# Kernel optimization log

Hardware: AMD Instinct MI355X
Metric: run time of the kernel (lower is better)

The kernel has to match this reference:

```python
import jax, jax.numpy as jnp
import numpy as np

B, S, H, M = 4, 4096, 2048, 64
LN_EPS = 1e-5


def setup_inputs() -> dict:
    key = jax.random.key(0)
    ks = jax.random.split(key, 12)
    rn = lambda i, shape, s: (jax.random.normal(ks[i], shape, jnp.float32) * s)
    return {
        "current_hidden_states": rn(0, (B, S, H), 1.0),
        "layer_input": rn(1, (B, S, H), 1.0),
        "memory_keys": rn(2, (M, H), 0.02),
        "memory_values": rn(3, (M, H), 0.02),
        "Wq": rn(4, (H, H), 0.02), "bq": jnp.zeros((H,), jnp.float32),
        "Wk": rn(5, (H, H), 0.02), "bk": jnp.zeros((H,), jnp.float32),
        "Wv": rn(6, (H, H), 0.02), "bv": jnp.zeros((H,), jnp.float32),
        "Wg1": rn(7, (H // 2, 2 * H), 0.02), "bg1": jnp.zeros((H // 2,), jnp.float32),
        "Wg2": rn(8, (1, H // 2), 0.02), "bg2": jnp.zeros((1,), jnp.float32),
        "ln_gamma": jnp.ones((H,), jnp.float32),
        "ln_beta": jnp.zeros((H,), jnp.float32),
        "usage_count": jnp.zeros((M,), jnp.int32),
        "timestamp": jnp.zeros((M,), jnp.int32),
    }


def _linear(x, W, b):
    # torch nn.Linear: y = x @ W.T + b, W is [out, in]
    return jnp.einsum("...i,oi->...o", x, W) + b


def reference(current_hidden_states, layer_input, memory_keys, memory_values,
              Wq, bq, Wk, bk, Wv, bv, Wg1, bg1, Wg2, bg2, ln_gamma, ln_beta,
              usage_count, timestamp):
    q = _linear(layer_input, Wq, bq)              # [B,S,H]
    k = _linear(current_hidden_states, Wk, bk)    # [B,S,H]
    v = _linear(current_hidden_states, Wv, bv)    # [B,S,H]

    # memory retrieval: softmax over the 64 memory slots
    attn = jax.nn.softmax(jnp.einsum("bsh,mh->bsm", q, memory_keys), axis=-1)
    retrieved = jnp.einsum("bsm,mh->bsh", attn, memory_values)

    # gated fusion
    combined = jnp.concatenate([layer_input, retrieved], axis=-1)  # [B,S,2H]
    g_hidden = jax.nn.relu(_linear(combined, Wg1, bg1))
    reuse_gate = jax.nn.sigmoid(_linear(g_hidden, Wg2, bg2))       # [B,S,1]
    fused = (1.0 - reuse_gate) * current_hidden_states + reuse_gate * retrieved

    # LayerNorm (dropout p=0 -> identity)
    mu = jnp.mean(fused, axis=-1, keepdims=True)
    var = jnp.mean(jnp.square(fused - mu), axis=-1, keepdims=True)
    out = (fused - mu) * jax.lax.rsqrt(var + LN_EPS) * ln_gamma + ln_beta

    # sequential argmin-scatter memory update (torch no_grad loop -> lax.scan)
    key_batch = k.mean(axis=1)    # [B,H]
    value_batch = v.mean(axis=1)  # [B,H]

    def step(carry, kv):
        mk, mv, uc, ts = carry
        ki, vi = kv
        score = uc.astype(jnp.float32) + ts.astype(jnp.float32) * 0.1
        idx = jnp.argmin(score)
        mk = mk.at[idx].set(ki)
        mv = mv.at[idx].set(vi)
        uc = uc.at[idx].add(1)
        ts = ts.at[idx].set(ts.max() + 1)
        return (mk, mv, uc, ts), None

    (mk, mv, uc, ts), _ = jax.lax.scan(
        step, (memory_keys, memory_values, usage_count, timestamp),
        (key_batch, value_batch))

    return out, reuse_gate, mk, mv, uc, ts
```

## Files before the change

### kernel.cpp

```cpp
#include <hip/hip_runtime.h>
#include <hip/hip_bf16.h>
#include <stdint.h>

typedef __bf16 bf16;
typedef __bf16 bf16x8 __attribute__((ext_vector_type(8)));
typedef __bf16 bf16x4 __attribute__((ext_vector_type(4)));
typedef float  f32x4  __attribute__((ext_vector_type(4)));

#define DI __device__ __forceinline__

constexpr int ROWS = 4 * 4096;
constexpr int HH   = 2048;
constexpr int MM   = 64;
constexpr int NHID = 1024;
constexpr int NC   = 1152;

constexpr size_t O_OUT  = 0;
constexpr size_t O_GATE = (size_t)ROWS * HH;
constexpr size_t O_MK   = O_GATE + ROWS;
constexpr size_t O_MV   = O_MK + (size_t)MM * HH;
constexpr size_t O_UC   = O_MV + (size_t)MM * HH;
constexpr size_t O_TS   = O_UC + MM;

constexpr size_t WS_XLB  = 0;
constexpr size_t WS_C    = WS_XLB + (size_t)ROWS * HH * 2;
constexpr size_t WS_BMAT = WS_C + (size_t)ROWS * NC * 2;
constexpr size_t WS_WQT  = WS_BMAT + (size_t)NC * HH * 2;
constexpr size_t WS_W1B  = WS_WQT + (size_t)HH * HH * 2;
constexpr size_t WS_MKP  = WS_W1B + (size_t)NHID * HH * 2;
constexpr size_t WS_MVP  = WS_MKP + (size_t)128 * HH * 2;
constexpr size_t WS_Q2T  = WS_MVP + (size_t)128 * HH * 2;
constexpr size_t WS_PF   = WS_Q2T + (size_t)NHID * MM * 2;
constexpr size_t WS_Q2F  = WS_PF + (size_t)MM * HH * 4;
constexpr size_t WS_CVEC = WS_Q2F + (size_t)MM * NHID * 4;
constexpr size_t WS_XBAR = WS_CVEC + 64 * 4;
constexpr size_t WS_KB   = WS_XBAR + (size_t)4 * HH * 4;
constexpr size_t WS_VB   = WS_KB + (size_t)4 * HH * 4;
constexpr size_t WS_MVT  = WS_VB + (size_t)4 * HH * 4;

DI void gload16(const void* g, void* l) {
    __builtin_amdgcn_global_load_lds((__attribute__((address_space(1))) void*)g,
                                     (__attribute__((address_space(3))) void*)l,
                                     16, 0, 0);
}

DI bf16x8 cvt8(f32x4 a, f32x4 b) {
    bf16x8 v;
    v[0]=(bf16)a[0]; v[1]=(bf16)a[1]; v[2]=(bf16)a[2]; v[3]=(bf16)a[3];
    v[4]=(bf16)b[0]; v[5]=(bf16)b[1]; v[6]=(bf16)b[2]; v[7]=(bf16)b[3];
    return v;
}

DI float wave_sum(float v) {
#pragma unroll
    for (int off = 32; off; off >>= 1) v += __shfl_xor(v, off);
    return v;
}

template <bool SPLITK, bool REMAP>
__global__ __launch_bounds__(256)
void gemm_bt(const bf16* __restrict__ A, int lda,
             const bf16* __restrict__ Bt, int ldb,
             void* __restrict__ Cv, int ldc,
             int Mmax, int kit)
{
    __shared__ __align__(16) bf16 As[128 * 64];
    __shared__ __align__(16) bf16 Bs[128 * 64];
    const int tid  = threadIdx.x;
    const int wid  = tid >> 6, lane = tid & 63;
    int bx, by;
    if (REMAP) {
        int bid = blockIdx.x;
        int xcd = bid & 7, loc = bid >> 3;
        bx = xcd * 16 + loc / 9;
        by = loc % 9;
    } else { bx = blockIdx.x; by = blockIdx.y; }
    const int m0   = bx * 128, n0 = by * 128;
    const int wr   = wid >> 1, wc = wid & 1;
    const int kt0  = blockIdx.z * kit;
    const int srow  = lane >> 3;
    const int sslot = (lane & 7) ^ srow;

    f32x4 acc[4][4] = {};

    for (int kt = kt0; kt < kt0 + kit; ++kt) {
        const bf16* Ak = A + (size_t)kt * 64;
        const bf16* Bk = Bt + (size_t)kt * 64;
#pragma unroll
        for (int c = 0; c < 4; ++c) {
            int ch  = wid * 4 + c;
            int row = ch * 8 + srow;
            gload16(Ak + (size_t)(m0 + row) * lda + sslot * 8, As + ch * 512);
        }
#pragma unroll
        for (int c = 0; c < 4; ++c) {
            int ch  = wid * 4 + c;
            int row = ch * 8 + srow;
            gload16(Bk + (size_t)(n0 + row) * ldb + sslot * 8, Bs + ch * 512);
        }
        __syncthreads();
#pragma unroll
        for (int ks = 0; ks < 2; ++ks) {
            bf16x8 av[4], bv[4];
#pragma unroll
            for (int mi = 0; mi < 4; ++mi) {
                int r = wr * 64 + mi * 16 + (lane & 15);
                int slot = ((ks * 4 + (lane >> 4)) ^ (r & 7)) * 8;
                av[mi] = *(const bf16x8*)&As[r * 64 + slot];
            }
#pragma unroll
            for (int ni = 0; ni < 4; ++ni) {
                int r = wc * 64 + ni * 16 + (lane & 15);
                int slot = ((ks * 4 + (lane >> 4)) ^ (r & 7)) * 8;
                bv[ni] = *(const bf16x8*)&Bs[r * 64 + slot];
            }
#pragma unroll
            for (int mi = 0; mi < 4; ++mi)
#pragma unroll
                for (int ni = 0; ni < 4; ++ni)
                    acc[mi][ni] = __builtin_amdgcn_mfma_f32_16x16x32_bf16(
                        av[mi], bv[ni], acc[mi][ni], 0, 0, 0);
        }
        __syncthreads();
    }

#pragma unroll
    for (int mi = 0; mi < 4; ++mi) {
#pragma unroll
        for (int ni = 0; ni < 4; ++ni) {
            int col = n0 + wc * 64 + ni * 16 + (lane & 15);
#pragma unroll
            for (int j = 0; j < 4; ++j) {
                int row = m0 + wr * 64 + mi * 16 + (lane >> 4) * 4 + j;
                if (row < Mmax) {
                    if (SPLITK)
                        atomicAdd((float*)Cv + (size_t)row * ldc + col, acc[mi][ni][j]);
                    else
                        ((bf16*)Cv)[(size_t)row * ldc + col] = (bf16)acc[mi][ni][j];
                }
            }
        }
    }
}

__global__ __launch_bounds__(256)
void conv_xl_k(const float* __restrict__ xl, bf16* __restrict__ xlb)
{
    size_t idx = ((size_t)blockIdx.x * 256 + threadIdx.x) * 8;
    f32x4 a = *(const f32x4*)&xl[idx];
    f32x4 b = *(const f32x4*)&xl[idx + 4];
    *(bf16x8*)&xlb[idx] = cvt8(a, b);
}

__global__ __launch_bounds__(256)
void transpose_k(const float* __restrict__ src, bf16* __restrict__ dst)
{
    __shared__ float T[64][72];
    const int o0 = blockIdx.y * 64, i0 = blockIdx.x * 64;
    const int t = threadIdx.x, r = t >> 3, c8 = (t & 7) * 8;
#pragma unroll
    for (int rep = 0; rep < 2; ++rep) {
        int row = r + rep * 32;
        *(f32x4*)&T[row][c8]     = *(const f32x4*)&src[(size_t)(o0 + row) * HH + i0 + c8];
        *(f32x4*)&T[row][c8 + 4] = *(const f32x4*)&src[(size_t)(o0 + row) * HH + i0 + c8 + 4];
    }
    __syncthreads();
#pragma unroll
    for (int rep = 0; rep < 2; ++rep) {
        int irow = r + rep * 32;
        bf16x8 v;
#pragma unroll
        for (int jj = 0; jj < 8; ++jj) v[jj] = (bf16)T[c8 + jj][irow];
        *(bf16x8*)&dst[(size_t)(i0 + irow) * HH + o0 + c8] = v;
    }
}

__global__ __launch_bounds__(256)
void padcpy_k(const float* __restrict__ mk, const float* __restrict__ mv,
              bf16* __restrict__ mkP, bf16* __restrict__ mvP)
{
    int idx = (blockIdx.x * 256 + threadIdx.x) * 8;
    const int half = 128 * HH;
    const float* s; bf16* d; int i;
    if (idx < half) { i = idx; d = mkP; s = mk; }
    else            { i = idx - half; d = mvP; s = mv; }
    bf16x8 v = {};
    if (i < MM * HH) {
        f32x4 a = *(const f32x4*)&s[i];
        f32x4 b = *(const f32x4*)&s[i + 4];
        v = cvt8(a, b);
    }
    *(bf16x8*)&d[i] = v;
}

__global__ __launch_bounds__(256)
void bmatfill_k(const float* __restrict__ Wg1, bf16* __restrict__ Bmat, bf16* __restrict__ W1b)
{
    int row = 64 + blockIdx.x;
    int c8  = threadIdx.x * 8;
    int j   = row - 64;
    bf16x8 v = {};
    if (j < NHID) {
        f32x4 a = *(const f32x4*)&Wg1[(size_t)j * 4096 + c8];
        f32x4 b = *(const f32x4*)&Wg1[(size_t)j * 4096 + c8 + 4];
        v = cvt8(a, b);
        f32x4 c = *(const f32x4*)&Wg1[(size_t)j * 4096 + 2048 + c8];
        f32x4 d = *(const f32x4*)&Wg1[(size_t)j * 4096 + 2048 + c8 + 4];
        *(bf16x8*)&W1b[(size_t)j * HH + c8] = cvt8(c, d);
    }
    *(bf16x8*)&Bmat[(size_t)row * HH + c8] = v;
}

__global__ __launch_bounds__(256)
void cvec_k(const float* __restrict__ bq, const float* __restrict__ mk, float* __restrict__ cvec)
{
    __shared__ float wS[4];
    const int m = blockIdx.x, t = threadIdx.x, wid = t >> 6, lane = t & 63;
    const int o0 = t * 8;
    f32x4 b0 = *(const f32x4*)&bq[o0];
    f32x4 b1 = *(const f32x4*)&bq[o0 + 4];
    f32x4 k0 = *(const f32x4*)&mk[(size_t)m * HH + o0];
    f32x4 k1 = *(const f32x4*)&mk[(size_t)m * HH + o0 + 4];
    float acc = b0[0]*k0[0] + b0[1]*k0[1] + b0[2]*k0[2] + b0[3]*k0[3]
              + b1[0]*k1[0] + b1[1]*k1[1] + b1[2]*k1[2] + b1[3]*k1[3];
    acc = wave_sum(acc);
    if (lane == 0) wS[wid] = acc;
    __syncthreads();
    if (t == 0) cvec[m] = wS[0] + wS[1] + wS[2] + wS[3];
}

__global__ __launch_bounds__(256)
void convp_k(const float* __restrict__ Pf, bf16* __restrict__ Bmat)
{
    int idx = (blockIdx.x * 256 + threadIdx.x) * 8;
    f32x4 a = *(const f32x4*)&Pf[idx];
    f32x4 b = *(const f32x4*)&Pf[idx + 4];
    *(bf16x8*)&Bmat[idx] = cvt8(a, b);
}

__global__ __launch_bounds__(256)
void trans_small_k(const float* __restrict__ Q2f, const float* __restrict__ mv,
                   bf16* __restrict__ q2t, bf16* __restrict__ mvT)
{
    int idx = blockIdx.x * 256 + threadIdx.x;
    if (idx < NHID * MM) {
        int j = idx >> 6, m = idx & 63;
        q2t[idx] = (bf16)Q2f[(size_t)m * NHID + j];
    } else {
        int i = idx - NHID * MM;
        int h = i >> 6, m = i & 63;
        mvT[i] = (bf16)mv[(size_t)m * HH + h];
    }
}

__global__ __launch_bounds__(256)
void epi_k(const bf16* __restrict__ Cb, const float* __restrict__ cvec,
           const bf16* __restrict__ mvT, const bf16* __restrict__ q2t,
           const float* __restrict__ chs,
           const float* __restrict__ bg1, const float* __restrict__ w2,
           const float* __restrict__ bg2,
           const float* __restrict__ gamma, const float* __restrict__ beta,
           float* __restrict__ out, bf16* __restrict__ xpart)
{
    __shared__ __align__(16) bf16 attnB[16 * 64];
    __shared__ float redA[4][16], redB[4][16];
    __shared__ float gS[16], muS[16], rsS[16];
    const int t = threadIdx.x, wid = t >> 6, lane = t & 63;
    const size_t row0 = (size_t)blockIdx.x * 16;
    const int cl = lane & 15;
    const int rbase = (lane >> 4) * 4;

    {
        float cv = cvec[lane];
#pragma unroll
        for (int rr = 0; rr < 4; ++rr) {
            int r = wid * 4 + rr;
            float s = (float)Cb[(row0 + r) * NC + lane] + cv;
            float mx = s;
#pragma unroll
            for (int off = 32; off; off >>= 1) mx = fmaxf(mx, __shfl_xor(mx, off));
            float e = expf(s - mx);
            float sum = e;
#pragma unroll
            for (int off = 32; off; off >>= 1) sum += __shfl_xor(sum, off);
            attnB[r * 64 + lane] = (bf16)(e / sum);
        }
    }
    __syncthreads();

    bf16x8 av0 = *(const bf16x8*)&attnB[cl * 64 +  0 + (lane >> 4) * 8];
    bf16x8 av1 = *(const bf16x8*)&attnB[cl * 64 + 32 + (lane >> 4) * 8];

    {
        float gp[4] = {};
        for (int nt = 0; nt < 16; ++nt) {
            int ct = wid * 256 + nt * 16 + cl;
            f32x4 acc = {};
            bf16x8 bv0 = *(const bf16x8*)&q2t[(size_t)ct * 64 +  0 + (lane >> 4) * 8];
            bf16x8 bv1 = *(const bf16x8*)&q2t[(size_t)ct * 64 + 32 + (lane >> 4) * 8];
            acc = __builtin_amdgcn_mfma_f32_16x16x32_bf16(av0, bv0, acc, 0, 0, 0);
            acc = __builtin_amdgcn_mfma_f32_16x16x32_bf16(av1, bv1, acc, 0, 0, 0);
            float b1 = bg1[ct], wv = w2[ct];
#pragma unroll
            for (int j = 0; j < 4; ++j) {
                float c = (float)Cb[(row0 + rbase + j) * NC + 64 + ct];
                float h = fmaxf(c + b1 + acc[j], 0.f);
                gp[j] += h * wv;
            }
        }
#pragma unroll
        for (int j = 0; j < 4; ++j) {
            gp[j] += __shfl_xor(gp[j], 1);
            gp[j] += __shfl_xor(gp[j], 2);
            gp[j] += __shfl_xor(gp[j], 4);
            gp[j] += __shfl_xor(gp[j], 8);
        }
        if (cl == 0) {
#pragma unroll
            for (int j = 0; j < 4; ++j) redA[wid][rbase + j] = gp[j];
        }
    }
    __syncthreads();
    if (t < 16) {
        float g = redA[0][t] + redA[1][t] + redA[2][t] + redA[3][t];
        g = 1.f / (1.f + expf(-(g + bg2[0])));
        gS[t] = g;
        out[O_GATE + row0 + t] = g;
    }
    __syncthreads();

    float gR[4], omR[4];
#pragma unroll
    for (int j = 0; j < 4; ++j) { gR[j] = gS[rbase + j]; omR[j] = 1.f - gR[j]; }

    {
        float sA[4] = {}, qA[4] = {};
        for (int nt = 0; nt < 32; ++nt) {
            int ct = wid * 512 + nt * 16 + cl;
            f32x4 acc = {};
            bf16x8 bv0 = *(const bf16x8*)&mvT[(size_t)ct * 64 +  0 + (lane >> 4) * 8];
            bf16x8 bv1 = *(const bf16x8*)&mvT[(size_t)ct * 64 + 32 + (lane >> 4) * 8];
            acc = __builtin_amdgcn_mfma_f32_16x16x32_bf16(av0, bv0, acc, 0, 0, 0);
            acc = __builtin_amdgcn_mfma_f32_16x16x32_bf16(av1, bv1, acc, 0, 0, 0);
            float xc = 0.f;
#pragma unroll
            for (int j = 0; j < 4; ++j) {
                float xv = chs[(row0 + rbase + j) * HH + ct];
                xc += xv;
                float fz = omR[j] * xv + gR[j] * acc[j];
                sA[j] += fz; qA[j] += fz * fz;
            }
            xc += __shfl_xor(xc, 16);
            xc += __shfl_xor(xc, 32);
            if (lane < 16) xpart[(size_t)blockIdx.x * 2048 + ct] = (bf16)xc;
        }
#pragma unroll
        for (int j = 0; j < 4; ++j) {
            sA[j] += __shfl_xor(sA[j], 1); qA[j] += __shfl_xor(qA[j], 1);
            sA[j] += __shfl_xor(sA[j], 2); qA[j] += __shfl_xor(qA[j], 2);
            sA[j] += __shfl_xor(sA[j], 4); qA[j] += __shfl_xor(qA[j], 4);
            sA[j] += __shfl_xor(sA[j], 8); qA[j] += __shfl_xor(qA[j], 8);
        }
        if (cl == 0) {
#pragma unroll
            for (int j = 0; j < 4; ++j) { redA[wid][rbase + j] = sA[j]; redB[wid][rbase + j] = qA[j]; }
        }
    }
    __syncthreads();
    if (t < 16) {
        float s = redA[0][t] + redA[1][t] + redA[2][t] + redA[3][t];
        float q = redB[0][t] + redB[1][t] + redB[2][t] + redB[3][t];
        float mu  = s * (1.f / 2048.f);
        float var = q * (1.f / 2048.f) - mu * mu;
        muS[t] = mu;
        rsS[t] = rsqrtf(var + 1e-5f);
    }
    __syncthreads();

    float muR[4], rsR[4];
#pragma unroll
    for (int j = 0; j < 4; ++j) { muR[j] = muS[rbase + j]; rsR[j] = rsS[rbase + j]; }

    for (int nt = 0; nt < 32; ++nt) {
        int ct = wid * 512 + nt * 16 + cl;
        f32x4 acc = {};
        bf16x8 bv0 = *(const bf16x8*)&mvT[(size_t)ct * 64 +  0 + (lane >> 4) * 8];
        bf16x8 bv1 = *(const bf16x8*)&mvT[(size_t)ct * 64 + 32 + (lane >> 4) * 8];
        acc = __builtin_amdgcn_mfma_f32_16x16x32_bf16(av0, bv0, acc, 0, 0, 0);
        acc = __builtin_amdgcn_mfma_f32_16x16x32_bf16(av1, bv1, acc, 0, 0, 0);
        float ga = gamma[ct], be = beta[ct];
#pragma unroll
        for (int j = 0; j < 4; ++j) {
            float xv = chs[(row0 + rbase + j) * HH + ct];
            float fz = omR[j] * xv + gR[j] * acc[j];
            out[O_OUT + (row0 + rbase + j) * HH + ct] = (fz - muR[j]) * rsR[j] * ga + be;
        }
    }
}

__global__ __launch_bounds__(256)
void xred_k(const bf16* __restrict__ xpart, float* __restrict__ xbar)
{
    int o = blockIdx.x * 256 + threadIdx.x;
    int b = o >> 11, h = o & 2047;
    const bf16* p = xpart + (size_t)(b * 256) * 2048 + h;
    float acc = 0.f;
    for (int k = 0; k < 256; ++k) acc += (float)p[(size_t)k * 2048];
    xbar[o] = acc;
}

__global__ __launch_bounds__(256)
void kbvb_k(const float* __restrict__ xbar,
            const float* __restrict__ Wk, const float* __restrict__ bk,
            const float* __restrict__ Wv, const float* __restrict__ bv,
            float* __restrict__ kb, float* __restrict__ vb)
{
    int gt = blockIdx.x * 256 + threadIdx.x;
    int out_idx = gt >> 2, part = gt & 3;
    int mat = out_idx >> 13, rem = out_idx & 8191;
    int b = rem >> 11, h = rem & 2047;
    const float* W    = mat ? Wv : Wk;
    const float* bias = mat ? bv : bk;
    const float* x    = xbar + b * HH;
    float acc = 0.f;
    const int i0 = part * 512;
    for (int i = i0; i < i0 + 512; i += 8) {
        f32x4 w0 = *(const f32x4*)&W[(size_t)h * HH + i];
        f32x4 w1 = *(const f32x4*)&W[(size_t)h * HH + i + 4];
        f32x4 x0 = *(const f32x4*)&x[i];
        f32x4 x1 = *(const f32x4*)&x[i + 4];
        acc += x0[0]*w0[0] + x0[1]*w0[1] + x0[2]*w0[2] + x0[3]*w0[3];
        acc += x1[0]*w1[0] + x1[1]*w1[1] + x1[2]*w1[2] + x1[3]*w1[3];
    }
    acc += __shfl_xor(acc, 1);
    acc += __shfl_xor(acc, 2);
    if (part == 0)
        (mat ? vb : kb)[b * HH + h] = bias[h] + acc * (1.f / 4096.f);
}

__global__ __launch_bounds__(256)
void copy_mkmv_k(const float* __restrict__ mk, const float* __restrict__ mv, float* __restrict__ out)
{
    int idx = (blockIdx.x * 256 + threadIdx.x) * 4;
    const int half = MM * HH;
    if (idx < half)
        *(f32x4*)&out[O_MK + idx] = *(const f32x4*)&mk[idx];
    else
        *(f32x4*)&out[O_MV + (idx - half)] = *(const f32x4*)&mv[idx - half];
}

__global__ __launch_bounds__(256)
void scan_k(const int* __restrict__ uc_in, const int* __restrict__ ts_in,
            const float* __restrict__ kb, const float* __restrict__ vb,
            float* __restrict__ out)
{
    __shared__ int ucS[64], tsS[64];
    __shared__ int idxS, tmaxS;
    const int t = threadIdx.x;
    if (t < 64) { ucS[t] = uc_in[t]; tsS[t] = ts_in[t]; }
    __syncthreads();
    for (int b = 0; b < 4; ++b) {
        if (t < 64) {
            float bs = (float)ucS[t] + 0.1f * (float)tsS[t];
            int bi = t;
            int tm = tsS[t];
#pragma unroll
            for (int off = 1; off < 64; off <<= 1) {
                float os = __shfl_xor(bs, off);
                int   oi = __shfl_xor(bi, off);
                int   om = __shfl_xor(tm, off);
                if (os < bs || (os == bs && oi < bi)) { bs = os; bi = oi; }
                tm = max(tm, om);
            }
            if (t == 0) { idxS = bi; tmaxS = tm; }
        }
        __syncthreads();
        int idx = idxS;
        int e = t * 8;
        *(f32x4*)&out[O_MK + (size_t)idx * HH + e]     = *(const f32x4*)&kb[b * HH + e];
        *(f32x4*)&out[O_MK + (size_t)idx * HH + e + 4] = *(const f32x4*)&kb[b * HH + e + 4];
        *(f32x4*)&out[O_MV + (size_t)idx * HH + e]     = *(const f32x4*)&vb[b * HH + e];
        *(f32x4*)&out[O_MV + (size_t)idx * HH + e + 4] = *(const f32x4*)&vb[b * HH + e + 4];
        __syncthreads();
        if (t == 0) { ucS[idx] += 1; tsS[idx] = tmaxS + 1; }
        __syncthreads();
    }
    if (t < 64) {
        out[O_UC + t] = (float)ucS[t];
        out[O_TS + t] = (float)tsS[t];
    }
}

extern "C" void kernel_launch(void* const* d_in, const int* in_sizes, int n_in,
                              void* d_out, int out_size, void* d_ws, size_t ws_size,
                              hipStream_t stream)
{
    const float* chs = (const float*)d_in[0];
    const float* xl  = (const float*)d_in[1];
    const float* mk  = (const float*)d_in[2];
    const float* mv  = (const float*)d_in[3];
    const float* Wq  = (const float*)d_in[4];
    const float* bq  = (const float*)d_in[5];
    const float* Wk  = (const float*)d_in[6];
    const float* bk  = (const float*)d_in[7];
    const float* Wv  = (const float*)d_in[8];
    const float* bv  = (const float*)d_in[9];
    const float* Wg1 = (const float*)d_in[10];
    const float* bg1 = (const float*)d_in[11];
    const float* Wg2 = (const float*)d_in[12];
    const float* bg2 = (const float*)d_in[13];
    const float* lng = (const float*)d_in[14];
    const float* lnb = (const float*)d_in[15];
    const int*   ucI = (const int*)d_in[16];
    const int*   tsI = (const int*)d_in[17];

    uint8_t* ws = (uint8_t*)d_ws;
    float* outp = (float*)d_out;

    bf16*  xlb  = (bf16*)(ws + WS_XLB);
    bf16*  xpart= (bf16*)(ws + WS_XLB);
    bf16*  Cb   = (bf16*)(ws + WS_C);
    bf16*  Bmat = (bf16*)(ws + WS_BMAT);
    bf16*  WqT  = (bf16*)(ws + WS_WQT);
    bf16*  W1b  = (bf16*)(ws + WS_W1B);
    bf16*  mkP  = (bf16*)(ws + WS_MKP);
    bf16*  mvP  = (bf16*)(ws + WS_MVP);
    bf16*  q2t  = (bf16*)(ws + WS_Q2T);
    bf16*  mvT  = (bf16*)(ws + WS_MVT);
    float* Pf   = (float*)(ws + WS_PF);
    float* Q2f  = (float*)(ws + WS_Q2F);
    float* cvec = (float*)(ws + WS_CVEC);
    float* xbar = (float*)(ws + WS_XBAR);
    float* kb   = (float*)(ws + WS_KB);
    float* vb   = (float*)(ws + WS_VB);

    hipMemsetAsync(Pf, 0, (size_t)MM * HH * 4, stream);
    hipMemsetAsync(Q2f, 0, (size_t)MM * NHID * 4, stream);

    conv_xl_k<<<16384, 256, 0, stream>>>(xl, xlb);
    transpose_k<<<dim3(32, 32), 256, 0, stream>>>(Wq, WqT);
    padcpy_k<<<256, 256, 0, stream>>>(mk, mv, mkP, mvP);
    bmatfill_k<<<1088, 256, 0, stream>>>(Wg1, Bmat, W1b);
    cvec_k<<<64, 256, 0, stream>>>(bq, mk, cvec);

    gemm_bt<true, false><<<dim3(1, 16, 8), 256, 0, stream>>>(mkP, HH, WqT, HH, Pf, HH, MM, 4);
    gemm_bt<true, false><<<dim3(1, 8, 8), 256, 0, stream>>>(mvP, HH, W1b, HH, Q2f, NHID, MM, 4);
    convp_k<<<64, 256, 0, stream>>>(Pf, Bmat);
    trans_small_k<<<768, 256, 0, stream>>>(Q2f, mv, q2t, mvT);

    gemm_bt<false, true><<<1152, 256, 0, stream>>>(xlb, HH, Bmat, HH, Cb, NC, ROWS, 32);

    epi_k<<<1024, 256, 0, stream>>>(Cb, cvec, mvT, q2t, chs, bg1, Wg2, bg2, lng, lnb, outp, xpart);

    xred_k<<<32, 256, 0, stream>>>(xpart, xbar);
    kbvb_k<<<256, 256, 0, stream>>>(xbar, Wk, bk, Wv, bv, kb, vb);
    copy_mkmv_k<<<256, 256, 0, stream>>>(mk, mv, outp);
    scan_k<<<1, 256, 0, stream>>>(ucI, tsI, kb, vb, outp);
}
```

Before: 369.8 us.

## Cache fused values in registers for LayerNorm pass and merge prep kernels

```diff
diff --git a/kernel.cpp b/kernel.cpp
--- a/kernel.cpp
+++ b/kernel.cpp
@@ -230,30 +230,28 @@
 }
 
 __global__ __launch_bounds__(256)
-void convp_k(const float* __restrict__ Pf, bf16* __restrict__ Bmat)
-{
-    int idx = (blockIdx.x * 256 + threadIdx.x) * 8;
-    f32x4 a = *(const f32x4*)&Pf[idx];
-    f32x4 b = *(const f32x4*)&Pf[idx + 4];
-    *(bf16x8*)&Bmat[idx] = cvt8(a, b);
-}
-
-__global__ __launch_bounds__(256)
-void trans_small_k(const float* __restrict__ Q2f, const float* __restrict__ mv,
-                   bf16* __restrict__ q2t, bf16* __restrict__ mvT)
-{
-    int idx = blockIdx.x * 256 + threadIdx.x;
-    if (idx < NHID * MM) {
+void prep2_k(const float* __restrict__ Pf, bf16* __restrict__ Bmat,
+             const float* __restrict__ Q2f, const float* __restrict__ mv,
+             bf16* __restrict__ q2t, bf16* __restrict__ mvT)
+{
+    int gid = blockIdx.x * 256 + threadIdx.x;
+    if (gid < 16384) {
+        int idx = gid * 8;
+        f32x4 a = *(const f32x4*)&Pf[idx];
+        f32x4 b = *(const f32x4*)&Pf[idx + 4];
+        *(bf16x8*)&Bmat[idx] = cvt8(a, b);
+    } else if (gid < 16384 + NHID * MM) {
+        int idx = gid - 16384;
         int j = idx >> 6, m = idx & 63;
         q2t[idx] = (bf16)Q2f[(size_t)m * NHID + j];
     } else {
-        int i = idx - NHID * MM;
+        int i = gid - 16384 - NHID * MM;
         int h = i >> 6, m = i & 63;
         mvT[i] = (bf16)mv[(size_t)m * HH + h];
     }
 }
 
-__global__ __launch_bounds__(256)
+__global__ __launch_bounds__(256, 4)
 void epi_k(const bf16* __restrict__ Cb, const float* __restrict__ cvec,
            const bf16* __restrict__ mvT, const bf16* __restrict__ q2t,
            const float* __restrict__ chs,
@@ -293,6 +291,7 @@
 
     {
         float gp[4] = {};
+#pragma unroll
         for (int nt = 0; nt < 16; ++nt) {
             int ct = wid * 256 + nt * 16 + cl;
             f32x4 acc = {};
@@ -333,8 +332,10 @@
 #pragma unroll
     for (int j = 0; j < 4; ++j) { gR[j] = gS[rbase + j]; omR[j] = 1.f - gR[j]; }
 
+    bf16x4 fzv[32];
     {
         float sA[4] = {}, qA[4] = {};
+#pragma unroll
         for (int nt = 0; nt < 32; ++nt) {
             int ct = wid * 512 + nt * 16 + cl;
             f32x4 acc = {};
@@ -348,6 +349,7 @@
                 float xv = chs[(row0 + rbase + j) * HH + ct];
                 xc += xv;
                 float fz = omR[j] * xv + gR[j] * acc[j];
+                fzv[nt][j] = (bf16)fz;
                 sA[j] += fz; qA[j] += fz * fz;
             }
             xc += __shfl_xor(xc, 16);
@@ -381,18 +383,13 @@
 #pragma unroll
     for (int j = 0; j < 4; ++j) { muR[j] = muS[rbase + j]; rsR[j] = rsS[rbase + j]; }
 
+#pragma unroll
     for (int nt = 0; nt < 32; ++nt) {
         int ct = wid * 512 + nt * 16 + cl;
-        f32x4 acc = {};
-        bf16x8 bv0 = *(const bf16x8*)&mvT[(size_t)ct * 64 +  0 + (lane >> 4) * 8];
-        bf16x8 bv1 = *(const bf16x8*)&mvT[(size_t)ct * 64 + 32 + (lane >> 4) * 8];
-        acc = __builtin_amdgcn_mfma_f32_16x16x32_bf16(av0, bv0, acc, 0, 0, 0);
-        acc = __builtin_amdgcn_mfma_f32_16x16x32_bf16(av1, bv1, acc, 0, 0, 0);
         float ga = gamma[ct], be = beta[ct];
 #pragma unroll
         for (int j = 0; j < 4; ++j) {
-            float xv = chs[(row0 + rbase + j) * HH + ct];
-            float fz = omR[j] * xv + gR[j] * acc[j];
+            float fz = (float)fzv[nt][j];
             out[O_OUT + (row0 + rbase + j) * HH + ct] = (fz - muR[j]) * rsR[j] * ga + be;
         }
     }
@@ -545,8 +542,7 @@
 
     gemm_bt<true, false><<<dim3(1, 16, 8), 256, 0, stream>>>(mkP, HH, WqT, HH, Pf, HH, MM, 4);
     gemm_bt<true, false><<<dim3(1, 8, 8), 256, 0, stream>>>(mvP, HH, W1b, HH, Q2f, NHID, MM, 4);
-    convp_k<<<64, 256, 0, stream>>>(Pf, Bmat);
-    trans_small_k<<<768, 256, 0, stream>>>(Q2f, mv, q2t, mvT);
+    prep2_k<<<832, 256, 0, stream>>>(Pf, Bmat, Q2f, mv, q2t, mvT);
 
     gemm_bt<false, true><<<1152, 256, 0, stream>>>(xlb, HH, Bmat, HH, Cb, NC, ROWS, 32);
 
```

Measured after the change: 495.7 us. +34.0%, slower.
